# Kernel tuning notes

Measured on AMD Instinct MI355X. Metric: run time of the kernel, lower is better.

Reference implementation:

```python
import jax, jax.numpy as jnp
import numpy as np
from jax import lax

B, S = 64, 256            # batch, max_seq_len
EMB = 1024                # embed (== decoder_hidden, required by outs buffer)
ENC = 512                 # encoder_hidden; 2*ENC = 1024
DEC = 1024                # decoder_hidden
GIN = EMB + 2 * ENC       # GRUCell input size = 2048


def setup_inputs() -> dict:
    key = jax.random.key(0)
    ks = jax.random.split(key, 12)
    w = 0.02
    inp = {
        "input": jax.random.normal(ks[0], (B, S, EMB), jnp.float32),
        "hidden": jax.random.normal(ks[1], (DEC, B), jnp.float32),  # [decoder_hidden, batch]
        "encoder_outs": jax.random.normal(ks[2], (B, S, 2 * ENC), jnp.float32),
        "lengths": jnp.maximum(jax.random.randint(ks[3], (B,), 0, S), 1).astype(jnp.int32),
        # Attention params (additive / Bahdanau): v^T tanh(W_enc*enc + W_dec*h)
        "W_enc": jax.random.normal(ks[4], (2 * ENC, DEC), jnp.float32) * w,
        "W_dec": jax.random.normal(ks[5], (DEC, DEC), jnp.float32) * w,
        "v": jax.random.normal(ks[6], (DEC,), jnp.float32) * w,
        # GRUCell params (torch layout: W_ih [3H, GIN], W_hh [3H, H])
        "W_ih": jax.random.normal(ks[7], (3 * DEC, GIN), jnp.float32) * w,
        "W_hh": jax.random.normal(ks[8], (3 * DEC, DEC), jnp.float32) * w,
        "b_ih": jax.random.normal(ks[9], (3 * DEC,), jnp.float32) * w,
        "b_hh": jax.random.normal(ks[10], (3 * DEC,), jnp.float32) * w,
    }
    return inp


def reference(input, hidden, encoder_outs, lengths, W_enc, W_dec, v, W_ih, W_hh, b_ih, b_hh):
    h0 = hidden.T                                  # [B, DEC]
    mask = jnp.arange(S)[None, :] < lengths[:, None]   # [B, S]
    enc_proj = encoder_outs @ W_enc                # [B, S, DEC] (hoisted out of the loop)

    # One shared teacher-forcing coin flip per timestep (torch.rand(1) < 0.5),
    # made deterministic with a fixed key.
    tf_flags = jax.random.uniform(jax.random.key(1), (S - 1,)) < 0.5

    def attention(h):
        # energy: [B, S]
        energy = jnp.tanh(enc_proj + (h @ W_dec)[:, None, :]) @ v
        energy = jnp.where(mask, energy, jnp.float32(-1e9))
        attn = jax.nn.softmax(energy, axis=1)
        return jnp.einsum("bs,bse->be", attn, encoder_outs)  # [B, 2*ENC]

    def gru_cell(x, h):
        gi = x @ W_ih.T + b_ih                     # [B, 3*DEC]
        gh = h @ W_hh.T + b_hh
        i_r, i_z, i_n = jnp.split(gi, 3, axis=1)
        h_r, h_z, h_n = jnp.split(gh, 3, axis=1)
        r = jax.nn.sigmoid(i_r + h_r)
        z = jax.nn.sigmoid(i_z + h_z)
        n = jnp.tanh(i_n + r * h_n)
        return (1.0 - z) * n + z * h

    # teacher inputs for step t are input[:, t-1, :], t = 1..S-1
    teach_seq = jnp.swapaxes(input, 0, 1)[: S - 1]  # [S-1, B, EMB]

    def step(carry, xt):
        h, prev = carry
        teach, tf = xt
        ctx = attention(h)
        sel = jnp.where(tf, teach, prev)            # scalar bool broadcast
        h_new = gru_cell(jnp.concatenate([sel, ctx], axis=1), h)
        return (h_new, h_new), h_new

    (_, _), hs = lax.scan(step, (h0, input[:, 0, :]), (teach_seq, tf_flags))
    outs = jnp.concatenate([input[:, 0:1, :], jnp.swapaxes(hs, 0, 1)], axis=1)  # [B, S, DEC]
    return outs
```

## Files before the change

### kernel.cpp

```cpp
#include <hip/hip_runtime.h>
#include <stdint.h>

typedef unsigned short u16;
typedef unsigned int   u32;
typedef unsigned long long u64;
typedef __attribute__((ext_vector_type(8))) short short8;
typedef __attribute__((ext_vector_type(4))) short s16x4;
typedef __attribute__((ext_vector_type(4))) float f32x4;

#define MFMA(a,b,c) __builtin_amdgcn_mfma_f32_16x16x32_bf16((a),(b),(c),0,0,0)
#define NBLK 256
#define NTHR 256
#define SMEM_BYTES 160832

static const long kOutB = 256*1024;

__device__ __forceinline__ float b2f(u16 v){ union{u32 u; float f;} c; c.u = ((u32)v)<<16; return c.f; }
__device__ __forceinline__ u16 f2b(float f){ union{float f; u32 u;} c; c.f = f; u32 r = c.u + 0x7FFFu + ((c.u>>16)&1u); return (u16)(r>>16); }
__device__ __forceinline__ float fexp2(float x){ return __builtin_amdgcn_exp2f(x); }
__device__ __forceinline__ float frcp(float x){ return __builtin_amdgcn_rcpf(x); }
__device__ __forceinline__ float tanh_(float x){ float e = fexp2(x*2.885390081777927f); return 1.f - 2.f*frcp(e+1.f); }
__device__ __forceinline__ float sigm_(float x){ return frcp(1.f + fexp2(-1.4426950408889634f*x)); }

__device__ __forceinline__ u64 ald64(const void* p){
    return __hip_atomic_load((const u64*)p, __ATOMIC_RELAXED, __HIP_MEMORY_SCOPE_AGENT);
}
__device__ __forceinline__ u32 ald32(const void* p){
    return __hip_atomic_load((const u32*)p, __ATOMIC_RELAXED, __HIP_MEMORY_SCOPE_AGENT);
}
__device__ __forceinline__ void ast64(void* p, u64 v){
    __hip_atomic_store((u64*)p, v, __ATOMIC_RELAXED, __HIP_MEMORY_SCOPE_AGENT);
}
__device__ __forceinline__ void ast32(void* p, u32 v){
    __hip_atomic_store((u32*)p, v, __ATOMIC_RELAXED, __HIP_MEMORY_SCOPE_AGENT);
}

__device__ __forceinline__ u32 rotl32_(u32 x, int r){ return (x << r) | (x >> (32 - r)); }
__device__ bool tf_bit(u32 j){
    const u32 k0 = 0u, k1 = 1u, k2 = 0x1BD11BDAu ^ 0u ^ 1u;
    const int R0[4] = {13,15,26,6}, R1[4] = {17,29,16,24};
    u32 x0 = 0u, x1 = j;
    x0 += k0; x1 += k1;
    for(int i=0;i<4;i++){ x0 += x1; x1 = rotl32_(x1,R0[i]); x1 ^= x0; }
    x0 += k1; x1 += k2 + 1u;
    for(int i=0;i<4;i++){ x0 += x1; x1 = rotl32_(x1,R1[i]); x1 ^= x0; }
    x0 += k2; x1 += k0 + 2u;
    for(int i=0;i<4;i++){ x0 += x1; x1 = rotl32_(x1,R0[i]); x1 ^= x0; }
    x0 += k0; x1 += k1 + 3u;
    for(int i=0;i<4;i++){ x0 += x1; x1 = rotl32_(x1,R1[i]); x1 ^= x0; }
    x0 += k1; x1 += k2 + 4u;
    for(int i=0;i<4;i++){ x0 += x1; x1 = rotl32_(x1,R0[i]); x1 ^= x0; }
    x0 += k2; x1 += k0 + 5u;
    return (((x0 ^ x1) >> 31) == 0u);
}

__device__ __forceinline__ void gridbar(u32* sync){
    asm volatile("s_waitcnt vmcnt(0)" ::: "memory");
    __syncthreads();
    if(threadIdx.x == 0){
        u32* cnt  = sync;
        u32* gen  = sync + 32;
        u32* gcnt = sync + 64 + (blockIdx.x >> 5)*32;
        u32 g = __hip_atomic_load(gen, __ATOMIC_RELAXED, __HIP_MEMORY_SCOPE_AGENT);
        u32 a = __hip_atomic_fetch_add(gcnt, 1u, __ATOMIC_RELAXED, __HIP_MEMORY_SCOPE_AGENT);
        bool done = false;
        if(a == 31u){
            __hip_atomic_store(gcnt, 0u, __ATOMIC_RELAXED, __HIP_MEMORY_SCOPE_AGENT);
            asm volatile("s_waitcnt vmcnt(0)" ::: "memory");
            u32 b = __hip_atomic_fetch_add(cnt, 1u, __ATOMIC_RELAXED, __HIP_MEMORY_SCOPE_AGENT);
            if(b == 7u){
                __hip_atomic_store(cnt, 0u, __ATOMIC_RELAXED, __HIP_MEMORY_SCOPE_AGENT);
                asm volatile("s_waitcnt vmcnt(0)" ::: "memory");
                __hip_atomic_store(gen, g + 1u, __ATOMIC_RELAXED, __HIP_MEMORY_SCOPE_AGENT);
                done = true;
            }
        }
        if(!done)
            while(__hip_atomic_load(gen, __ATOMIC_RELAXED, __HIP_MEMORY_SCOPE_AGENT) == g)
                __builtin_amdgcn_s_sleep(1);
    }
    __syncthreads();
}

__global__ void k_cvt(const float* __restrict__ in, u16* __restrict__ out, int n){
    int i = blockIdx.x*blockDim.x + threadIdx.x;
    int st = gridDim.x*blockDim.x;
    for(; i < n; i += st) out[i] = f2b(in[i]);
}

__global__ void k_cvt_t(const float* __restrict__ in, u16* __restrict__ out, int R, int C){
    __shared__ float tile[32][33];
    int bx = blockIdx.x, by = blockIdx.y;
    int tx = threadIdx.x, ty = threadIdx.y;
    for(int j = 0; j < 32; j += 8) tile[ty+j][tx] = in[(by*32+ty+j)*C + bx*32+tx];
    __syncthreads();
    for(int j = 0; j < 32; j += 8) out[(bx*32+ty+j)*R + by*32+tx] = f2b(tile[tx][ty+j]);
}

__global__ void k_init(const float* __restrict__ hidden, const float* __restrict__ input,
                       float* __restrict__ h0f, u16* __restrict__ h0b, float* __restrict__ out,
                       u32* __restrict__ sync){
    int i = blockIdx.x*blockDim.x + threadIdx.x;
    int b = i >> 10, d = i & 1023;
    float h = hidden[d*64 + b];
    h0f[i] = h; h0b[i] = f2b(h);
    out[(long)b*kOutB + d] = input[(long)b*kOutB + d];
    if(i < 512) sync[i] = 0u;
}

__global__ __launch_bounds__(256) void k_gemm_ep(const u16* __restrict__ A, const u16* __restrict__ BT,
                                                 u16* __restrict__ Cb){
    int m0 = blockIdx.x*64, n0 = blockIdx.y*64;
    int w = threadIdx.x >> 6, l = threadIdx.x & 63;
    int r0 = l & 15, kh = (l >> 4) * 8;
    const u16* arow = A + (long)(m0 + w*16 + r0)*1024 + kh;
    f32x4 acc[4] = {};
    for(int k0 = 0; k0 < 1024; k0 += 32){
        short8 a = *(const short8*)(arow + k0);
        #pragma unroll
        for(int j = 0; j < 4; ++j){
            short8 b = *(const short8*)(BT + (long)(n0 + j*16 + r0)*1024 + k0 + kh);
            acc[j] = MFMA(a, b, acc[j]);
        }
    }
    int orow = m0 + w*16 + (l>>4)*4;
    int ocol = n0 + (l & 15);
    #pragma unroll
    for(int j = 0; j < 4; ++j)
        #pragma unroll
        for(int r = 0; r < 4; ++r)
            Cb[(long)(orow + r)*1024 + ocol + j*16] = f2b(acc[j][r]);
}

__global__ __launch_bounds__(NTHR, 1) void k_steps(
        const u16* __restrict__ epb, const float* __restrict__ input, const u16* __restrict__ encb,
        const u16* __restrict__ wihb, const u16* __restrict__ whhb, const u16* __restrict__ wdecT,
        const float* __restrict__ bih, const float* __restrict__ bhh,
        const float* __restrict__ vv, const int* __restrict__ lengths,
        float* __restrict__ hW, float* __restrict__ eny,
        u16* __restrict__ crot, const float* __restrict__ hf0, u16* __restrict__ hrot,
        float* __restrict__ out, u32* __restrict__ sync){
    extern __shared__ char smem[];
    u16*   s_ep = (u16*)smem;
    float* sB   = (float*)(smem + 131072);
    float* sA   = (float*)(smem + 135168);
    float* sRed = (float*)(smem + 136192);
    f32x4* sAcc = (f32x4*)(smem + 136256);

    const int bid = blockIdx.x, tid = threadIdx.x;
    const int w = tid >> 6, l = tid & 63;
    const int r0 = l & 15, kh = (l >> 4) * 8;
    const int rg = bid >> 6, cg = bid & 63;
    const int p2_b = bid >> 2, p2_sq = bid & 3;

    const int p2_len = lengths[p2_b];
    float rv[16];
    #pragma unroll
    for(int j = 0; j < 16; ++j) rv[j] = vv[l*16 + j];

    {
        const u16* src = epb + (long)(p2_b*256 + p2_sq*64)*1024;
        for(int i = tid; i < 8192; i += NTHR)
            *(short8*)(s_ep + i*8) = *(const short8*)(src + i*8);
    }
    __syncthreads();

    const u16* p1_brow = wdecT + (long)(cg*16 + r0)*1024 + w*256 + kh;
    const long p1_aoff = (long)(rg*16 + r0)*1024 + w*256 + kh;
    const int kxb = w*512, khb = w*256;
    const u16* b_wr = wihb + (long)(       cg*16 + r0)*2048 + kxb + kh;
    const u16* b_wz = wihb + (long)(1024 + cg*16 + r0)*2048 + kxb + kh;
    const u16* b_wn = wihb + (long)(2048 + cg*16 + r0)*2048 + kxb + kh;
    const u16* b_vr = whhb + (long)(       cg*16 + r0)*1024 + khb + kh;
    const u16* b_vz = whhb + (long)(1024 + cg*16 + r0)*1024 + khb + kh;
    const u16* b_vn = whhb + (long)(2048 + cg*16 + r0)*1024 + khb + kh;
    const long a_row_off = (long)(rg*16 + r0)*1024;
    const float* g_inf = input + (long)(rg*16 + r0)*kOutB;
    const int ucol = cg*16 + (l & 15);
    const float bir = bih[ucol], biz = bih[1024+ucol], bin_ = bih[2048+ucol];
    const float bhr = bhh[ucol], bhz = bhh[1024+ucol], bhn = bhh[2048+ucol];
    const int erow = rg*16 + (l>>4)*4;
    float hold[4];
    #pragma unroll
    for(int r = 0; r < 4; ++r) hold[r] = hf0[(erow + r)*1024 + ucol];

    for(int t = 1; t < 256; ++t){
        const u16* hbo = hrot + (size_t)(t-1)*65536;
        u16*       hbn = hrot + (size_t)t*65536;
        u16*       ctxt = crot + (size_t)(t-1)*65536;
        {
            const u16* arow = hbo + p1_aoff;
            f32x4 acc = {};
            #pragma unroll
            for(int k0 = 0; k0 < 256; k0 += 32)
                acc = MFMA(*(const short8*)(arow + k0), *(const short8*)(p1_brow + k0), acc);
            sAcc[w*64 + l] = acc;
            __syncthreads();
            if(w == 0){
                f32x4 s = sAcc[l];
                s += sAcc[64 + l]; s += sAcc[128 + l]; s += sAcc[192 + l];
                #pragma unroll
                for(int r = 0; r < 4; ++r){
                    float mine = s[r];
                    float oth = __shfl_xor(mine, 1);
                    if(!(l & 1)){
                        union{ float f[2]; u64 q; } pk; pk.f[0] = mine; pk.f[1] = oth;
                        ast64(hW + (erow + r)*1024 + cg*16 + (l & 15), pk.q);
                    }
                }
            }
        }
        gridbar(sync);
        {
            float rh[16];
            const float* hp = hW + p2_b*1024 + l*16;
            #pragma unroll
            for(int j = 0; j < 8; ++j){
                union{ u64 q; float f[2]; } uu; uu.q = ald64(hp + j*2);
                rh[2*j] = uu.f[0]; rh[2*j+1] = uu.f[1];
            }
            const u16* lrow = s_ep + (w*16)*1024 + l*16;
            for(int si = 0; si < 16; ++si){
                int s = p2_sq*64 + w*16 + si;
                short8 q0 = *(const short8*)(lrow + si*1024);
                short8 q1 = *(const short8*)(lrow + si*1024 + 8);
                float acc = 0.f;
                #pragma unroll
                for(int j = 0; j < 8; ++j) acc += rv[j]   * tanh_(b2f((u16)q0[j]) + rh[j]);
                #pragma unroll
                for(int j = 0; j < 8; ++j) acc += rv[8+j] * tanh_(b2f((u16)q1[j]) + rh[8+j]);
                #pragma unroll
                for(int off = 32; off; off >>= 1) acc += __shfl_xor(acc, off);
                if(l == 0){
                    float val = (s < p2_len) ? acc : -1e9f;
                    ast32(eny + p2_b*256 + s, __float_as_uint(val));
                }
            }
        }
        gridbar(sync);
        {
            float e = __uint_as_float(ald32(eny + p2_b*256 + tid));
            float m = e;
            #pragma unroll
            for(int off = 32; off; off >>= 1) m = fmaxf(m, __shfl_xor(m, off));
            if(l == 0) sRed[w] = m;
            __syncthreads();
            m = fmaxf(fmaxf(sRed[0], sRed[1]), fmaxf(sRed[2], sRed[3]));
            float pp = fexp2((e - m)*1.4426950408889634f);
            sA[tid] = pp;
            float sm = pp;
            #pragma unroll
            for(int off = 32; off; off >>= 1) sm += __shfl_xor(sm, off);
            if(l == 0) sRed[4 + w] = sm;
            __syncthreads();
            float inv = 1.f / (sRed[4] + sRed[5] + sRed[6] + sRed[7]);
            const u16* eb = encb + (long)p2_b*262144 + p2_sq*256 + l*4;
            float a0=0.f, a1=0.f, a2=0.f, a3=0.f;
            #pragma unroll 4
            for(int si = 0; si < 64; ++si){
                int s = w*64 + si;
                float ps = sA[s];
                s16x4 q = *(const s16x4*)(eb + (long)s*1024);
                a0 += ps*b2f((u16)q[0]); a1 += ps*b2f((u16)q[1]);
                a2 += ps*b2f((u16)q[2]); a3 += ps*b2f((u16)q[3]);
            }
            sB[w*256 + l*4+0] = a0; sB[w*256 + l*4+1] = a1;
            sB[w*256 + l*4+2] = a2; sB[w*256 + l*4+3] = a3;
            __syncthreads();
            float c = (sB[tid] + sB[256+tid] + sB[512+tid] + sB[768+tid]) * inv;
            u32 cb = (u32)f2b(c);
            u32 ob = (u32)__shfl_xor((int)cb, 1);
            if(!(tid & 1))
                ast32((u32*)ctxt + ((p2_b*1024 + p2_sq*256 + tid) >> 1), cb | (ob << 16));
        }
        gridbar(sync);
        {
            const bool useTeach = (t == 1) || tf_bit((u32)(t - 1));
            f32x4 a_r = {}, a_z = {}, a_n = {};
            if(w < 2){
                if(useTeach){
                    const float* sf = g_inf + (long)(t - 1)*1024 + kxb + kh;
                    for(int k0 = 0; k0 < 512; k0 += 32){
                        f32x4 u0q = *(const f32x4*)(sf + k0);
                        f32x4 u1q = *(const f32x4*)(sf + k0 + 4);
                        short8 a;
                        a[0]=(short)f2b(u0q.x); a[1]=(short)f2b(u0q.y);
                        a[2]=(short)f2b(u0q.z); a[3]=(short)f2b(u0q.w);
                        a[4]=(short)f2b(u1q.x); a[5]=(short)f2b(u1q.y);
                        a[6]=(short)f2b(u1q.z); a[7]=(short)f2b(u1q.w);
                        a_r = MFMA(a, *(const short8*)(b_wr + k0), a_r);
                        a_z = MFMA(a, *(const short8*)(b_wz + k0), a_z);
                        a_n = MFMA(a, *(const short8*)(b_wn + k0), a_n);
                    }
                } else {
                    const u16* ar = hbo + a_row_off + kxb + kh;
                    for(int k0 = 0; k0 < 512; k0 += 32){
                        short8 a = *(const short8*)(ar + k0);
                        a_r = MFMA(a, *(const short8*)(b_wr + k0), a_r);
                        a_z = MFMA(a, *(const short8*)(b_wz + k0), a_z);
                        a_n = MFMA(a, *(const short8*)(b_wn + k0), a_n);
                    }
                }
            } else {
                const u16* ar = ctxt + a_row_off + (kxb - 1024) + kh;
                for(int k0 = 0; k0 < 512; k0 += 32){
                    short8 a = *(const short8*)(ar + k0);
                    a_r = MFMA(a, *(const short8*)(b_wr + k0), a_r);
                    a_z = MFMA(a, *(const short8*)(b_wz + k0), a_z);
                    a_n = MFMA(a, *(const short8*)(b_wn + k0), a_n);
                }
            }
            f32x4 h_r = {}, h_z = {}, h_n = {};
            {
                const u16* ah = hbo + a_row_off + khb + kh;
                #pragma unroll
                for(int k0 = 0; k0 < 256; k0 += 32){
                    short8 h = *(const short8*)(ah + k0);
                    h_r = MFMA(h, *(const short8*)(b_vr + k0), h_r);
                    h_z = MFMA(h, *(const short8*)(b_vz + k0), h_z);
                    h_n = MFMA(h, *(const short8*)(b_vn + k0), h_n);
                }
            }
            sAcc[(w*6+0)*64 + l] = a_r;
            sAcc[(w*6+1)*64 + l] = a_z;
            sAcc[(w*6+2)*64 + l] = a_n;
            sAcc[(w*6+3)*64 + l] = h_r;
            sAcc[(w*6+4)*64 + l] = h_z;
            sAcc[(w*6+5)*64 + l] = h_n;
            __syncthreads();
            if(w == 0){
                f32x4 air = sAcc[0*64+l] + sAcc[6*64+l] + sAcc[12*64+l] + sAcc[18*64+l];
                f32x4 aiz = sAcc[1*64+l] + sAcc[7*64+l] + sAcc[13*64+l] + sAcc[19*64+l];
                f32x4 ain = sAcc[2*64+l] + sAcc[8*64+l] + sAcc[14*64+l] + sAcc[20*64+l];
                f32x4 ahr = sAcc[3*64+l] + sAcc[9*64+l] + sAcc[15*64+l] + sAcc[21*64+l];
                f32x4 ahz = sAcc[4*64+l] + sAcc[10*64+l] + sAcc[16*64+l] + sAcc[22*64+l];
                f32x4 ahn = sAcc[5*64+l] + sAcc[11*64+l] + sAcc[17*64+l] + sAcc[23*64+l];
                #pragma unroll
                for(int r = 0; r < 4; ++r){
                    int b = erow + r;
                    float rgt = sigm_(air[r] + bir + ahr[r] + bhr);
                    float z   = sigm_(aiz[r] + biz + ahz[r] + bhz);
                    float n   = tanh_(ain[r] + bin_ + rgt*(ahn[r] + bhn));
                    float hn = (1.f - z)*n + z*hold[r];
                    hold[r] = hn;
                    out[(long)b*kOutB + (long)t*1024 + ucol] = hn;
                    u32 mb = (u32)f2b(hn);
                    u32 ob = (u32)__shfl_xor((int)mb, 1);
                    if(!(l & 1))
                        ast32((u32*)hbn + ((b*1024 + ucol) >> 1), mb | (ob << 16));
                }
            }
        }
        gridbar(sync);
    }
}

extern "C" void kernel_launch(void* const* d_in, const int* in_sizes, int n_in,
                              void* d_out, int out_size, void* d_ws, size_t ws_size,
                              hipStream_t stream){
    (void)in_sizes; (void)n_in; (void)out_size;
    const float* input    = (const float*)d_in[0];
    const float* hidden   = (const float*)d_in[1];
    const float* enc_outs = (const float*)d_in[2];
    const int*   lengths  = (const int*)  d_in[3];
    const float* W_enc    = (const float*)d_in[4];
    const float* W_dec    = (const float*)d_in[5];
    const float* v        = (const float*)d_in[6];
    const float* W_ih     = (const float*)d_in[7];
    const float* W_hh     = (const float*)d_in[8];
    const float* b_ih     = (const float*)d_in[9];
    const float* b_hh     = (const float*)d_in[10];
    float* out = (float*)d_out;

    char* p = (char*)d_ws;
    auto alloc = [&](size_t bytes){ void* r = (void*)p; p += (bytes + 255) & ~(size_t)255; return r; };
    u16* epb   = (u16*)alloc((size_t)16384*1024*2);
    u16* encb  = (u16*)alloc((size_t)16384*1024*2);
    u16* wihb  = (u16*)alloc((size_t)3072*2048*2);
    u16* whhb  = (u16*)alloc((size_t)3072*1024*2);
    u16* wencT = (u16*)alloc((size_t)1024*1024*2);
    u16* wdecT = (u16*)alloc((size_t)1024*1024*2);
    float* hf0 = (float*)alloc((size_t)64*1024*4);
    u16* hrot  = (u16*)alloc((size_t)256*65536*2);
    u16* crot  = (u16*)alloc((size_t)255*65536*2);
    float* hW  = (float*)alloc((size_t)64*1024*4);
    float* eny = (float*)alloc((size_t)64*256*4);
    u32* sync  = (u32*)alloc(2048);
    if((size_t)(p - (char*)d_ws) > ws_size) return;

    k_cvt<<<2048, 256, 0, stream>>>(enc_outs, encb, 16384*1024);
    k_cvt<<<1024, 256, 0, stream>>>(W_ih,     wihb, 3072*2048);
    k_cvt<<<512,  256, 0, stream>>>(W_hh,     whhb, 3072*1024);
    k_cvt_t<<<dim3(32,32), dim3(32,8), 0, stream>>>(W_enc, wencT, 1024, 1024);
    k_cvt_t<<<dim3(32,32), dim3(32,8), 0, stream>>>(W_dec, wdecT, 1024, 1024);
    k_init<<<256, 256, 0, stream>>>(hidden, input, hf0, hrot, out, sync);
    k_gemm_ep<<<dim3(256,16), 256, 0, stream>>>(encb, wencT, epb);

    hipFuncSetAttribute((const void*)k_steps, hipFuncAttributeMaxDynamicSharedMemorySize, SMEM_BYTES);
    k_steps<<<NBLK, NTHR, SMEM_BYTES, stream>>>(epb, input, encb, wihb, whhb, wdecT,
                                                b_ih, b_hh, v, lengths,
                                                hW, eny, crot, hf0, hrot,
                                                out, sync);
}
```

Measured before the change: 10.54 ms.

## Keep GRU weight slices register-resident and pre-convert teacher inputs to bf16

Each block's slices of W_ih and W_hh are loaded once into registers before the time loop, so they are no longer refetched from global memory or L2 on every step. Teacher-forced inputs are converted to bf16 in a prep kernel, which removes the per-step fp32 load and conversion and lets both input branches share one unrolled MFMA loop. Output stores are marked nontemporal. The cost is about 144 extra VGPRs per thread, which risks spills, plus an extra conversion pass and a larger workspace.

Result: slower. 11.92 ms (+13.1%).

```diff
diff --git a/kernel.cpp b/kernel.cpp
--- a/kernel.cpp
+++ b/kernel.cpp
@@ -133,7 +133,7 @@
 }
 
 __global__ __launch_bounds__(NTHR, 1) void k_steps(
-        const u16* __restrict__ epb, const float* __restrict__ input, const u16* __restrict__ encb,
+        const u16* __restrict__ epb, const u16* __restrict__ inb, const u16* __restrict__ encb,
         const u16* __restrict__ wihb, const u16* __restrict__ whhb, const u16* __restrict__ wdecT,
         const float* __restrict__ bih, const float* __restrict__ bhh,
         const float* __restrict__ vv, const int* __restrict__ lengths,
@@ -175,7 +175,7 @@
     const u16* b_vz = whhb + (long)(1024 + cg*16 + r0)*1024 + khb + kh;
     const u16* b_vn = whhb + (long)(2048 + cg*16 + r0)*1024 + khb + kh;
     const long a_row_off = (long)(rg*16 + r0)*1024;
-    const float* g_inf = input + (long)(rg*16 + r0)*kOutB;
+    const u16* g_inb = inb + (long)(rg*16 + r0)*kOutB;
     const int ucol = cg*16 + (l & 15);
     const float bir = bih[ucol], biz = bih[1024+ucol], bin_ = bih[2048+ucol];
     const float bhr = bhh[ucol], bhz = bhh[1024+ucol], bhn = bhh[2048+ucol];
@@ -183,6 +183,21 @@
     float hold[4];
     #pragma unroll
     for(int r = 0; r < 4; ++r) hold[r] = hf0[(erow + r)*1024 + ucol];
+
+    short8 rwr[16], rwz[16], rwn[16];
+    short8 rvr[8],  rvz[8],  rvn[8];
+    #pragma unroll
+    for(int i = 0; i < 16; ++i){
+        rwr[i] = *(const short8*)(b_wr + i*32);
+        rwz[i] = *(const short8*)(b_wz + i*32);
+        rwn[i] = *(const short8*)(b_wn + i*32);
+    }
+    #pragma unroll
+    for(int i = 0; i < 8; ++i){
+        rvr[i] = *(const short8*)(b_vr + i*32);
+        rvz[i] = *(const short8*)(b_vz + i*32);
+        rvn[i] = *(const short8*)(b_vn + i*32);
+    }
 
     for(int t = 1; t < 256; ++t){
         const u16* hbo = hrot + (size_t)(t-1)*65536;
@@ -278,47 +293,34 @@
             const bool useTeach = (t == 1) || tf_bit((u32)(t - 1));
             f32x4 a_r = {}, a_z = {}, a_n = {};
             if(w < 2){
-                if(useTeach){
-                    const float* sf = g_inf + (long)(t - 1)*1024 + kxb + kh;
-                    for(int k0 = 0; k0 < 512; k0 += 32){
-                        f32x4 u0q = *(const f32x4*)(sf + k0);
-                        f32x4 u1q = *(const f32x4*)(sf + k0 + 4);
-                        short8 a;
-                        a[0]=(short)f2b(u0q.x); a[1]=(short)f2b(u0q.y);
-                        a[2]=(short)f2b(u0q.z); a[3]=(short)f2b(u0q.w);
-                        a[4]=(short)f2b(u1q.x); a[5]=(short)f2b(u1q.y);
-                        a[6]=(short)f2b(u1q.z); a[7]=(short)f2b(u1q.w);
-                        a_r = MFMA(a, *(const short8*)(b_wr + k0), a_r);
-                        a_z = MFMA(a, *(const short8*)(b_wz + k0), a_z);
-                        a_n = MFMA(a, *(const short8*)(b_wn + k0), a_n);
-                    }
-                } else {
-                    const u16* ar = hbo + a_row_off + kxb + kh;
-                    for(int k0 = 0; k0 < 512; k0 += 32){
-                        short8 a = *(const short8*)(ar + k0);
-                        a_r = MFMA(a, *(const short8*)(b_wr + k0), a_r);
-                        a_z = MFMA(a, *(const short8*)(b_wz + k0), a_z);
-                        a_n = MFMA(a, *(const short8*)(b_wn + k0), a_n);
-                    }
+                const u16* ar = useTeach ? (g_inb + (long)(t - 1)*1024 + kxb + kh)
+                                         : (hbo + a_row_off + kxb + kh);
+                #pragma unroll
+                for(int i = 0; i < 16; ++i){
+                    short8 a = *(const short8*)(ar + i*32);
+                    a_r = MFMA(a, rwr[i], a_r);
+                    a_z = MFMA(a, rwz[i], a_z);
+                    a_n = MFMA(a, rwn[i], a_n);
                 }
             } else {
                 const u16* ar = ctxt + a_row_off + (kxb - 1024) + kh;
-                for(int k0 = 0; k0 < 512; k0 += 32){
-                    short8 a = *(const short8*)(ar + k0);
-                    a_r = MFMA(a, *(const short8*)(b_wr + k0), a_r);
-                    a_z = MFMA(a, *(const short8*)(b_wz + k0), a_z);
-                    a_n = MFMA(a, *(const short8*)(b_wn + k0), a_n);
+                #pragma unroll
+                for(int i = 0; i < 16; ++i){
+                    short8 a = *(const short8*)(ar + i*32);
+                    a_r = MFMA(a, rwr[i], a_r);
+                    a_z = MFMA(a, rwz[i], a_z);
+                    a_n = MFMA(a, rwn[i], a_n);
                 }
             }
             f32x4 h_r = {}, h_z = {}, h_n = {};
             {
                 const u16* ah = hbo + a_row_off + khb + kh;
                 #pragma unroll
-                for(int k0 = 0; k0 < 256; k0 += 32){
-                    short8 h = *(const short8*)(ah + k0);
-                    h_r = MFMA(h, *(const short8*)(b_vr + k0), h_r);
-                    h_z = MFMA(h, *(const short8*)(b_vz + k0), h_z);
-                    h_n = MFMA(h, *(const short8*)(b_vn + k0), h_n);
+                for(int i = 0; i < 8; ++i){
+                    short8 h = *(const short8*)(ah + i*32);
+                    h_r = MFMA(h, rvr[i], h_r);
+                    h_z = MFMA(h, rvz[i], h_z);
+                    h_n = MFMA(h, rvn[i], h_n);
                 }
             }
             sAcc[(w*6+0)*64 + l] = a_r;
@@ -343,7 +345,7 @@
                     float n   = tanh_(ain[r] + bin_ + rgt*(ahn[r] + bhn));
                     float hn = (1.f - z)*n + z*hold[r];
                     hold[r] = hn;
-                    out[(long)b*kOutB + (long)t*1024 + ucol] = hn;
+                    __builtin_nontemporal_store(hn, &out[(long)b*kOutB + (long)t*1024 + ucol]);
                     u32 mb = (u32)f2b(hn);
                     u32 ob = (u32)__shfl_xor((int)mb, 1);
                     if(!(l & 1))
@@ -375,6 +377,7 @@
     char* p = (char*)d_ws;
     auto alloc = [&](size_t bytes){ void* r = (void*)p; p += (bytes + 255) & ~(size_t)255; return r; };
     u16* epb   = (u16*)alloc((size_t)16384*1024*2);
+    u16* inb   = (u16*)alloc((size_t)16384*1024*2);
     u16* encb  = (u16*)alloc((size_t)16384*1024*2);
     u16* wihb  = (u16*)alloc((size_t)3072*2048*2);
     u16* whhb  = (u16*)alloc((size_t)3072*1024*2);
@@ -389,6 +392,7 @@
     if((size_t)(p - (char*)d_ws) > ws_size) return;
 
     k_cvt<<<2048, 256, 0, stream>>>(enc_outs, encb, 16384*1024);
+    k_cvt<<<2048, 256, 0, stream>>>(input,    inb,  16384*1024);
     k_cvt<<<1024, 256, 0, stream>>>(W_ih,     wihb, 3072*2048);
     k_cvt<<<512,  256, 0, stream>>>(W_hh,     whhb, 3072*1024);
     k_cvt_t<<<dim3(32,32), dim3(32,8), 0, stream>>>(W_enc, wencT, 1024, 1024);
@@ -397,7 +401,7 @@
     k_gemm_ep<<<dim3(256,16), 256, 0, stream>>>(encb, wencT, epb);
 
     hipFuncSetAttribute((const void*)k_steps, hipFuncAttributeMaxDynamicSharedMemorySize, SMEM_BYTES);
-    k_steps<<<NBLK, NTHR, SMEM_BYTES, stream>>>(epb, input, encb, wihb, whhb, wdecT,
+    k_steps<<<NBLK, NTHR, SMEM_BYTES, stream>>>(epb, inb, encb, wihb, whhb, wdecT,
                                                 b_ih, b_hh, v, lengths,
                                                 hW, eny, crot, hf0, hrot,
                                                 out, sync);
```
